# Kernel optimization log

Hardware: AMD Instinct MI355X
Metric: run time of the kernel (lower is better)

## Reference

```python
import jax, jax.numpy as jnp
import numpy as np

Np_, Ny, Nu = 5, 8, 4
NZ = Np_ * (Ny + Nu)  # 60


def setup_inputs() -> dict:
    key = jax.random.key(0)
    ks = jax.random.split(key, 6)
    B, T = 8192, 1024
    u = jax.random.normal(ks[0], (B, T, Nu), dtype=jnp.float32)
    z0 = jax.random.normal(ks[1], (B, NZ), dtype=jnp.float32)
    W1 = jax.random.normal(ks[2], (NZ, 128), dtype=jnp.float32) * (1.0 / np.sqrt(NZ))
    b1 = jnp.zeros((128,), dtype=jnp.float32)
    W2 = jax.random.normal(ks[3], (128, 128), dtype=jnp.float32) * (1.0 / np.sqrt(128))
    b2 = jnp.zeros((128,), dtype=jnp.float32)
    W3 = jax.random.normal(ks[4], (128, Ny), dtype=jnp.float32) * (1.0 / np.sqrt(128))
    b3 = jnp.zeros((Ny,), dtype=jnp.float32)
    return {"u": u, "z0": z0, "W1": W1, "b1": b1, "W2": W2, "b2": b2,
            "W3": W3, "b3": b3}


def reference(u, z0, W1, b1, W2, b2, W3, b3):
    # u: [B, T, Nu], z0: [B, Np*(Ny+Nu)] -> y sequence [B, T, Ny]
    def step(z, u_t):
        h = jnp.tanh(z @ W1 + b1)
        h = jnp.tanh(h @ W2 + b2)
        y = h @ W3 + b3                      # [B, Ny]
        ypseq = z[:, : Np_ * Ny]
        upseq = z[:, Np_ * Ny:]
        z_new = jnp.concatenate(
            (ypseq[:, Ny:], y, upseq[:, Nu:], u_t), axis=-1)
        return z_new, y

    u_tbc = jnp.transpose(u, (1, 0, 2))      # [T, B, Nu]
    _, ys = jax.lax.scan(step, z0, u_tbc)    # ys: [T, B, Ny]
    return jnp.transpose(ys, (1, 0, 2))      # [B, T, Ny]
```

## Files before the change

kernel.cpp:

```cpp
#include <hip/hip_runtime.h>

#define T_STEPS 1024
#define NZV 60
#define H 128
#define NY 8
#define NU 4
#define ZSTR 72
#define HSTR 136

typedef __attribute__((ext_vector_type(8))) short bf16x8;
typedef __attribute__((ext_vector_type(4))) short bf16x4;
typedef __attribute__((ext_vector_type(4))) float f32x4;

__device__ __forceinline__ unsigned short f2bf(float x) {
    unsigned u = __float_as_uint(x);
    u += 0x7FFFu + ((u >> 16) & 1u);
    return (unsigned short)(u >> 16);
}

__device__ __forceinline__ float tanh_fast(float x) {
    float e = __builtin_amdgcn_exp2f(x * 2.8853900817779268f);
    return fmaf(-2.0f, __builtin_amdgcn_rcpf(e + 1.0f), 1.0f);
}

__global__ __launch_bounds__(256, 2)
void cstr_scan_kernel(const float* __restrict__ u_g, const float* __restrict__ z0_g,
                      const float* __restrict__ W1, const float* __restrict__ b1,
                      const float* __restrict__ W2, const float* __restrict__ b2,
                      const float* __restrict__ W3, const float* __restrict__ b3,
                      float* __restrict__ out) {
    __shared__ unsigned short zbuf[2][16][ZSTR];
    __shared__ unsigned short h1s[16][HSTR];
    __shared__ unsigned short h2s[16][HSTR];

    const int tid   = threadIdx.x;
    const int wid   = tid >> 6;
    const int lane  = tid & 63;
    const int b0    = blockIdx.x * 16;
    const int col   = lane & 15;
    const int kg    = lane >> 4;
    const int wrow0 = kg * 4;
    const int urow  = lane >> 2;
    const int uc    = lane & 3;
    const int n0    = wid * 2;

    bf16x8 w1f[2][2], w2f[4][2], w3f[4];
    float b1v[2], b2v[2], b3v;
#pragma unroll
    for (int nl = 0; nl < 2; ++nl) {
        b1v[nl] = b1[(n0 + nl) * 16 + col];
        b2v[nl] = b2[(n0 + nl) * 16 + col];
    }
    b3v = (col < NY) ? b3[col] : 0.f;

#pragma unroll
    for (int kc = 0; kc < 2; ++kc)
#pragma unroll
        for (int nl = 0; nl < 2; ++nl) {
            bf16x8 v;
#pragma unroll
            for (int j = 0; j < 8; ++j) {
                int k = kc * 32 + kg * 8 + j;
                float w = (k < NZV) ? W1[k * H + (n0 + nl) * 16 + col] : 0.f;
                v[j] = (short)f2bf(w);
            }
            w1f[kc][nl] = v;
        }
#pragma unroll
    for (int kc = 0; kc < 4; ++kc)
#pragma unroll
        for (int nl = 0; nl < 2; ++nl) {
            bf16x8 v;
#pragma unroll
            for (int j = 0; j < 8; ++j) {
                int k = kc * 32 + kg * 8 + j;
                v[j] = (short)f2bf(W2[k * H + (n0 + nl) * 16 + col]);
            }
            w2f[kc][nl] = v;
        }
#pragma unroll
    for (int kc = 0; kc < 4; ++kc) {
        bf16x8 v;
#pragma unroll
        for (int j = 0; j < 8; ++j) {
            int k = kc * 32 + kg * 8 + j;
            float w = (col < NY) ? W3[k * NY + col] : 0.f;
            v[j] = (short)f2bf(w);
        }
        w3f[kc] = v;
    }

    {
        unsigned short* zs = &zbuf[0][0][0];
        for (int i = tid; i < 2 * 16 * ZSTR; i += 256) zs[i] = 0;
        __syncthreads();
        for (int i = tid; i < 16 * NZV; i += 256) {
            int r = i / NZV, c = i - r * NZV;
            zbuf[0][r][c] = f2bf(z0_g[(size_t)(b0 + r) * NZV + c]);
        }
        __syncthreads();
    }

    float ureg = 0.f, ureg_n = 0.f;
    if (wid == 3)
        ureg = u_g[(size_t)(b0 + urow) * (T_STEPS * NU) + uc];

    f32x4 yprev = { 0.f, 0.f, 0.f, 0.f };

    int cur = 0;
#pragma unroll 1
    for (int t = 0; t < T_STEPS; ++t) {
        const int nxt = cur ^ 1;

        if (wid == 0 && t > 0 && col < NY) {
#pragma unroll
            for (int r = 0; r < 4; ++r)
                out[(size_t)(b0 + wrow0 + r) * (T_STEPS * NY) + (size_t)(t - 1) * NY + col] = yprev[r];
        }
        if (wid == 3 && t + 1 < T_STEPS)
            ureg_n = u_g[(size_t)(b0 + urow) * (T_STEPS * NU) + (size_t)(t + 1) * NU + uc];

        bf16x8 za[2];
#pragma unroll
        for (int kc = 0; kc < 2; ++kc)
            za[kc] = *(const bf16x8*)&zbuf[cur][col][kc * 32 + kg * 8];
        f32x4 c1[2];
#pragma unroll
        for (int nl = 0; nl < 2; ++nl) {
            f32x4 acc = { b1v[nl], b1v[nl], b1v[nl], b1v[nl] };
            acc = __builtin_amdgcn_mfma_f32_16x16x32_bf16(za[0], w1f[0][nl], acc, 0, 0, 0);
            acc = __builtin_amdgcn_mfma_f32_16x16x32_bf16(za[1], w1f[1][nl], acc, 0, 0, 0);
            c1[nl] = acc;
        }
#pragma unroll
        for (int nl = 0; nl < 2; ++nl)
#pragma unroll
            for (int r = 0; r < 4; ++r)
                h1s[wrow0 + r][(n0 + nl) * 16 + col] = f2bf(tanh_fast(c1[nl][r]));

        if (wid == 3) {
            bf16x4 m0 = *(const bf16x4*)&zbuf[cur][urow][8 + 8 * uc];
            bf16x4 m1 = *(const bf16x4*)&zbuf[cur][urow][12 + 8 * uc];
            bf16x4 m2 = *(const bf16x4*)&zbuf[cur][urow][44 + 4 * uc];
            *(bf16x4*)&zbuf[nxt][urow][8 * uc]      = m0;
            *(bf16x4*)&zbuf[nxt][urow][8 * uc + 4]  = m1;
            *(bf16x4*)&zbuf[nxt][urow][40 + 4 * uc] = m2;
            zbuf[nxt][urow][56 + uc] = f2bf(ureg);
        }
        __syncthreads();

        bf16x8 ha[4];
#pragma unroll
        for (int kc = 0; kc < 4; ++kc)
            ha[kc] = *(const bf16x8*)&h1s[col][kc * 32 + kg * 8];
        f32x4 c2[2];
#pragma unroll
        for (int nl = 0; nl < 2; ++nl) {
            f32x4 a0 = { b2v[nl], b2v[nl], b2v[nl], b2v[nl] };
            f32x4 a1 = { 0.f, 0.f, 0.f, 0.f };
            a0 = __builtin_amdgcn_mfma_f32_16x16x32_bf16(ha[0], w2f[0][nl], a0, 0, 0, 0);
            a1 = __builtin_amdgcn_mfma_f32_16x16x32_bf16(ha[1], w2f[1][nl], a1, 0, 0, 0);
            a0 = __builtin_amdgcn_mfma_f32_16x16x32_bf16(ha[2], w2f[2][nl], a0, 0, 0, 0);
            a1 = __builtin_amdgcn_mfma_f32_16x16x32_bf16(ha[3], w2f[3][nl], a1, 0, 0, 0);
            c2[nl] = a0 + a1;
        }
#pragma unroll
        for (int nl = 0; nl < 2; ++nl)
#pragma unroll
            for (int r = 0; r < 4; ++r)
                h2s[wrow0 + r][(n0 + nl) * 16 + col] = f2bf(tanh_fast(c2[nl][r]));
        __syncthreads();

        if (wid == 0) {
            bf16x8 h2a[4];
#pragma unroll
            for (int kc = 0; kc < 4; ++kc)
                h2a[kc] = *(const bf16x8*)&h2s[col][kc * 32 + kg * 8];
            f32x4 ya = { b3v, b3v, b3v, b3v };
            f32x4 yb = { 0.f, 0.f, 0.f, 0.f };
            ya = __builtin_amdgcn_mfma_f32_16x16x32_bf16(h2a[0], w3f[0], ya, 0, 0, 0);
            yb = __builtin_amdgcn_mfma_f32_16x16x32_bf16(h2a[1], w3f[1], yb, 0, 0, 0);
            ya = __builtin_amdgcn_mfma_f32_16x16x32_bf16(h2a[2], w3f[2], ya, 0, 0, 0);
            yb = __builtin_amdgcn_mfma_f32_16x16x32_bf16(h2a[3], w3f[3], yb, 0, 0, 0);
            f32x4 y = ya + yb;
            if (col < NY) {
#pragma unroll
                for (int r = 0; r < 4; ++r)
                    zbuf[nxt][wrow0 + r][32 + col] = f2bf(y[r]);
            }
            yprev = y;
        }
        __syncthreads();

        cur = nxt;
        ureg = ureg_n;
    }

    if (wid == 0 && (lane & 15) < NY) {
#pragma unroll
        for (int r = 0; r < 4; ++r)
            out[(size_t)(b0 + wrow0 + r) * (T_STEPS * NY) + (size_t)(T_STEPS - 1) * NY + (lane & 15)] = yprev[r];
    }
}

extern "C" void kernel_launch(void* const* d_in, const int* in_sizes, int n_in,
                              void* d_out, int out_size, void* d_ws, size_t ws_size,
                              hipStream_t stream) {
    (void)in_sizes; (void)n_in; (void)d_ws; (void)ws_size; (void)out_size;
    const float* u  = (const float*)d_in[0];
    const float* z0 = (const float*)d_in[1];
    const float* W1 = (const float*)d_in[2];
    const float* b1 = (const float*)d_in[3];
    const float* W2 = (const float*)d_in[4];
    const float* b2 = (const float*)d_in[5];
    const float* W3 = (const float*)d_in[6];
    const float* b3 = (const float*)d_in[7];
    float* out = (float*)d_out;

    dim3 grid(8192 / 16);
    dim3 block(256);
    cstr_scan_kernel<<<grid, block, 0, stream>>>(u, z0, W1, b1, W2, b2, W3, b3, out);
}
```

Baseline: 1.116 ms.

## Split hidden columns across 8 waves and distribute final layer as partial sums

Doubles the block to 512 threads so each of 8 waves owns one 16-column slice of the hidden layers, halving per-wave MFMA work on the serial critical path of each timestep. The output layer is no longer computed by wave 0 alone: every wave multiplies its own h2 slice against its slice of W3 and writes a partial sum to shared memory, which wave 0 then reduces. This shortens the per-step dependency chain at the cost of more waves contending at each barrier, an extra LDS reduction, and some wasted MFMA lanes (half-zero K inputs).

```diff
diff --git a/kernel.cpp b/kernel.cpp
--- a/kernel.cpp
+++ b/kernel.cpp
@@ -23,7 +23,7 @@
     return fmaf(-2.0f, __builtin_amdgcn_rcpf(e + 1.0f), 1.0f);
 }
 
-__global__ __launch_bounds__(256, 2)
+__global__ __launch_bounds__(512, 4)
 void cstr_scan_kernel(const float* __restrict__ u_g, const float* __restrict__ z0_g,
                       const float* __restrict__ W1, const float* __restrict__ b1,
                       const float* __restrict__ W2, const float* __restrict__ b2,
@@ -32,6 +32,7 @@
     __shared__ unsigned short zbuf[2][16][ZSTR];
     __shared__ unsigned short h1s[16][HSTR];
     __shared__ unsigned short h2s[16][HSTR];
+    __shared__ f32x4 ypart[8][64];
 
     const int tid   = threadIdx.x;
     const int wid   = tid >> 6;
@@ -42,59 +43,52 @@
     const int wrow0 = kg * 4;
     const int urow  = lane >> 2;
     const int uc    = lane & 3;
-    const int n0    = wid * 2;
-
-    bf16x8 w1f[2][2], w2f[4][2], w3f[4];
-    float b1v[2], b2v[2], b3v;
-#pragma unroll
-    for (int nl = 0; nl < 2; ++nl) {
-        b1v[nl] = b1[(n0 + nl) * 16 + col];
-        b2v[nl] = b2[(n0 + nl) * 16 + col];
-    }
-    b3v = (col < NY) ? b3[col] : 0.f;
-
-#pragma unroll
-    for (int kc = 0; kc < 2; ++kc)
-#pragma unroll
-        for (int nl = 0; nl < 2; ++nl) {
-            bf16x8 v;
+    const int nbase = wid * 16;
+
+    bf16x8 w1f[2], w2f[4], w3f;
+    const float b1v = b1[nbase + col];
+    const float b2v = b2[nbase + col];
+    const float b3seed = (wid == 0 && col < NY) ? b3[col] : 0.f;
+
+#pragma unroll
+    for (int kc = 0; kc < 2; ++kc) {
+        bf16x8 v;
+#pragma unroll
+        for (int j = 0; j < 8; ++j) {
+            int k = kc * 32 + kg * 8 + j;
+            float w = (k < NZV) ? W1[k * H + nbase + col] : 0.f;
+            v[j] = (short)f2bf(w);
+        }
+        w1f[kc] = v;
+    }
+#pragma unroll
+    for (int kc = 0; kc < 4; ++kc) {
+        bf16x8 v;
+#pragma unroll
+        for (int j = 0; j < 8; ++j) {
+            int k = kc * 32 + kg * 8 + j;
+            v[j] = (short)f2bf(W2[k * H + nbase + col]);
+        }
+        w2f[kc] = v;
+    }
+    {
+        bf16x8 v = { 0, 0, 0, 0, 0, 0, 0, 0 };
+        if (kg < 2) {
 #pragma unroll
             for (int j = 0; j < 8; ++j) {
-                int k = kc * 32 + kg * 8 + j;
-                float w = (k < NZV) ? W1[k * H + (n0 + nl) * 16 + col] : 0.f;
+                int k = nbase + kg * 8 + j;
+                float w = (col < NY) ? W3[k * NY + col] : 0.f;
                 v[j] = (short)f2bf(w);
             }
-            w1f[kc][nl] = v;
-        }
-#pragma unroll
-    for (int kc = 0; kc < 4; ++kc)
-#pragma unroll
-        for (int nl = 0; nl < 2; ++nl) {
-            bf16x8 v;
-#pragma unroll
-            for (int j = 0; j < 8; ++j) {
-                int k = kc * 32 + kg * 8 + j;
-                v[j] = (short)f2bf(W2[k * H + (n0 + nl) * 16 + col]);
-            }
-            w2f[kc][nl] = v;
-        }
-#pragma unroll
-    for (int kc = 0; kc < 4; ++kc) {
-        bf16x8 v;
-#pragma unroll
-        for (int j = 0; j < 8; ++j) {
-            int k = kc * 32 + kg * 8 + j;
-            float w = (col < NY) ? W3[k * NY + col] : 0.f;
-            v[j] = (short)f2bf(w);
-        }
-        w3f[kc] = v;
+        }
+        w3f = v;
     }
 
     {
         unsigned short* zs = &zbuf[0][0][0];
-        for (int i = tid; i < 2 * 16 * ZSTR; i += 256) zs[i] = 0;
-        __syncthreads();
-        for (int i = tid; i < 16 * NZV; i += 256) {
+        for (int i = tid; i < 2 * 16 * ZSTR; i += 512) zs[i] = 0;
+        __syncthreads();
+        for (int i = tid; i < 16 * NZV; i += 512) {
             int r = i / NZV, c = i - r * NZV;
             zbuf[0][r][c] = f2bf(z0_g[(size_t)(b0 + r) * NZV + c]);
         }
@@ -102,7 +96,7 @@
     }
 
     float ureg = 0.f, ureg_n = 0.f;
-    if (wid == 3)
+    if (wid == 7)
         ureg = u_g[(size_t)(b0 + urow) * (T_STEPS * NU) + uc];
 
     f32x4 yprev = { 0.f, 0.f, 0.f, 0.f };
@@ -117,28 +111,19 @@
             for (int r = 0; r < 4; ++r)
                 out[(size_t)(b0 + wrow0 + r) * (T_STEPS * NY) + (size_t)(t - 1) * NY + col] = yprev[r];
         }
-        if (wid == 3 && t + 1 < T_STEPS)
+        if (wid == 7 && t + 1 < T_STEPS)
             ureg_n = u_g[(size_t)(b0 + urow) * (T_STEPS * NU) + (size_t)(t + 1) * NU + uc];
 
-        bf16x8 za[2];
-#pragma unroll
-        for (int kc = 0; kc < 2; ++kc)
-            za[kc] = *(const bf16x8*)&zbuf[cur][col][kc * 32 + kg * 8];
-        f32x4 c1[2];
-#pragma unroll
-        for (int nl = 0; nl < 2; ++nl) {
-            f32x4 acc = { b1v[nl], b1v[nl], b1v[nl], b1v[nl] };
-            acc = __builtin_amdgcn_mfma_f32_16x16x32_bf16(za[0], w1f[0][nl], acc, 0, 0, 0);
-            acc = __builtin_amdgcn_mfma_f32_16x16x32_bf16(za[1], w1f[1][nl], acc, 0, 0, 0);
-            c1[nl] = acc;
-        }
-#pragma unroll
-        for (int nl = 0; nl < 2; ++nl)
-#pragma unroll
-            for (int r = 0; r < 4; ++r)
-                h1s[wrow0 + r][(n0 + nl) * 16 + col] = f2bf(tanh_fast(c1[nl][r]));
-
-        if (wid == 3) {
+        bf16x8 za0 = *(const bf16x8*)&zbuf[cur][col][kg * 8];
+        bf16x8 za1 = *(const bf16x8*)&zbuf[cur][col][32 + kg * 8];
+        f32x4 c1 = { b1v, b1v, b1v, b1v };
+        c1 = __builtin_amdgcn_mfma_f32_16x16x32_bf16(za0, w1f[0], c1, 0, 0, 0);
+        c1 = __builtin_amdgcn_mfma_f32_16x16x32_bf16(za1, w1f[1], c1, 0, 0, 0);
+#pragma unroll
+        for (int r = 0; r < 4; ++r)
+            h1s[wrow0 + r][nbase + col] = f2bf(tanh_fast(c1[r]));
+
+        if (wid == 7) {
             bf16x4 m0 = *(const bf16x4*)&zbuf[cur][urow][8 + 8 * uc];
             bf16x4 m1 = *(const bf16x4*)&zbuf[cur][urow][12 + 8 * uc];
             bf16x4 m2 = *(const bf16x4*)&zbuf[cur][urow][44 + 4 * uc];
@@ -149,46 +134,39 @@
         }
         __syncthreads();
 
-        bf16x8 ha[4];
-#pragma unroll
-        for (int kc = 0; kc < 4; ++kc)
-            ha[kc] = *(const bf16x8*)&h1s[col][kc * 32 + kg * 8];
-        f32x4 c2[2];
-#pragma unroll
-        for (int nl = 0; nl < 2; ++nl) {
-            f32x4 a0 = { b2v[nl], b2v[nl], b2v[nl], b2v[nl] };
-            f32x4 a1 = { 0.f, 0.f, 0.f, 0.f };
-            a0 = __builtin_amdgcn_mfma_f32_16x16x32_bf16(ha[0], w2f[0][nl], a0, 0, 0, 0);
-            a1 = __builtin_amdgcn_mfma_f32_16x16x32_bf16(ha[1], w2f[1][nl], a1, 0, 0, 0);
-            a0 = __builtin_amdgcn_mfma_f32_16x16x32_bf16(ha[2], w2f[2][nl], a0, 0, 0, 0);
-            a1 = __builtin_amdgcn_mfma_f32_16x16x32_bf16(ha[3], w2f[3][nl], a1, 0, 0, 0);
-            c2[nl] = a0 + a1;
-        }
-#pragma unroll
-        for (int nl = 0; nl < 2; ++nl)
-#pragma unroll
-            for (int r = 0; r < 4; ++r)
-                h2s[wrow0 + r][(n0 + nl) * 16 + col] = f2bf(tanh_fast(c2[nl][r]));
+        bf16x8 ha0 = *(const bf16x8*)&h1s[col][0 * 32 + kg * 8];
+        bf16x8 ha1 = *(const bf16x8*)&h1s[col][1 * 32 + kg * 8];
+        bf16x8 ha2 = *(const bf16x8*)&h1s[col][2 * 32 + kg * 8];
+        bf16x8 ha3 = *(const bf16x8*)&h1s[col][3 * 32 + kg * 8];
+        f32x4 a0 = { b2v, b2v, b2v, b2v };
+        f32x4 a1 = { 0.f, 0.f, 0.f, 0.f };
+        a0 = __builtin_amdgcn_mfma_f32_16x16x32_bf16(ha0, w2f[0], a0, 0, 0, 0);
+        a1 = __builtin_amdgcn_mfma_f32_16x16x32_bf16(ha1, w2f[1], a1, 0, 0, 0);
+        a0 = __builtin_amdgcn_mfma_f32_16x16x32_bf16(ha2, w2f[2], a0, 0, 0, 0);
+        a1 = __builtin_amdgcn_mfma_f32_16x16x32_bf16(ha3, w2f[3], a1, 0, 0, 0);
+        f32x4 c2 = a0 + a1;
+#pragma unroll
+        for (int r = 0; r < 4; ++r)
+            h2s[wrow0 + r][nbase + col] = f2bf(tanh_fast(c2[r]));
+
+        bf16x8 af = { 0, 0, 0, 0, 0, 0, 0, 0 };
+        if (kg < 2)
+            af = *(const bf16x8*)&h2s[col][nbase + kg * 8];
+        f32x4 yp = { b3seed, b3seed, b3seed, b3seed };
+        yp = __builtin_amdgcn_mfma_f32_16x16x32_bf16(af, w3f, yp, 0, 0, 0);
+        ypart[wid][lane] = yp;
         __syncthreads();
 
         if (wid == 0) {
-            bf16x8 h2a[4];
-#pragma unroll
-            for (int kc = 0; kc < 4; ++kc)
-                h2a[kc] = *(const bf16x8*)&h2s[col][kc * 32 + kg * 8];
-            f32x4 ya = { b3v, b3v, b3v, b3v };
-            f32x4 yb = { 0.f, 0.f, 0.f, 0.f };
-            ya = __builtin_amdgcn_mfma_f32_16x16x32_bf16(h2a[0], w3f[0], ya, 0, 0, 0);
-            yb = __builtin_amdgcn_mfma_f32_16x16x32_bf16(h2a[1], w3f[1], yb, 0, 0, 0);
-            ya = __builtin_amdgcn_mfma_f32_16x16x32_bf16(h2a[2], w3f[2], ya, 0, 0, 0);
-            yb = __builtin_amdgcn_mfma_f32_16x16x32_bf16(h2a[3], w3f[3], yb, 0, 0, 0);
-            f32x4 y = ya + yb;
+            f32x4 y = ypart[0][lane];
+#pragma unroll
+            for (int w = 1; w < 8; ++w) y = y + ypart[w][lane];
+            yprev = y;
             if (col < NY) {
 #pragma unroll
                 for (int r = 0; r < 4; ++r)
                     zbuf[nxt][wrow0 + r][32 + col] = f2bf(y[r]);
             }
-            yprev = y;
         }
         __syncthreads();
 
@@ -196,10 +174,10 @@
         ureg = ureg_n;
     }
 
-    if (wid == 0 && (lane & 15) < NY) {
+    if (wid == 0 && col < NY) {
 #pragma unroll
         for (int r = 0; r < 4; ++r)
-            out[(size_t)(b0 + wrow0 + r) * (T_STEPS * NY) + (size_t)(T_STEPS - 1) * NY + (lane & 15)] = yprev[r];
+            out[(size_t)(b0 + wrow0 + r) * (T_STEPS * NY) + (size_t)(T_STEPS - 1) * NY + col] = yprev[r];
     }
 }
 
@@ -218,6 +196,6 @@
     float* out = (float*)d_out;
 
     dim3 grid(8192 / 16);
-    dim3 block(256);
+    dim3 block(512);
     cstr_scan_kernel<<<grid, block, 0, stream>>>(u, z0, W1, b1, W2, b2, W3, b3, out);
 }
```

After: 1.288 ms. 15.4% more time.

## Fold output layer into next step's first layer to drop a barrier

Applied to the files above, without the earlier changes.

Precomputes W3·W1[y rows] as a fused weight so the first-layer pre-activation of step t reads the previous step's h2 directly, instead of waiting for y to be computed and written back into z. y is now computed off the critical path by wave 0, in parallel with the first-layer MFMAs. This cuts one __syncthreads per timestep (three to two). In exchange it adds MFMAs per step (K=128 instead of 8 for the y contribution) and a double-buffered h2 array, and the product W3·W1 rounded to bf16 changes numerics slightly.

```diff
diff --git a/kernel.cpp b/kernel.cpp
--- a/kernel.cpp
+++ b/kernel.cpp
@@ -31,7 +31,7 @@
                       float* __restrict__ out) {
     __shared__ unsigned short zbuf[2][16][ZSTR];
     __shared__ unsigned short h1s[16][HSTR];
-    __shared__ unsigned short h2s[16][HSTR];
+    __shared__ unsigned short h2s[2][16][HSTR];
 
     const int tid   = threadIdx.x;
     const int wid   = tid >> 6;
@@ -42,14 +42,19 @@
     const int wrow0 = kg * 4;
     const int urow  = lane >> 2;
     const int uc    = lane & 3;
-    const int n0    = wid * 2;
-
-    bf16x8 w1f[2][2], w2f[4][2], w3f[4];
-    float b1v[2], b2v[2], b3v;
+    const int nbase = wid * 32;
+
+    bf16x8 w1f[2][2], w1yx[2], w4f[4][2], w2f[4][2], w3f[4];
+    float b1v[2], b1e[2], b2v[2], b3v;
 #pragma unroll
     for (int nl = 0; nl < 2; ++nl) {
-        b1v[nl] = b1[(n0 + nl) * 16 + col];
-        b2v[nl] = b2[(n0 + nl) * 16 + col];
+        const int n = nbase + nl * 16 + col;
+        b1v[nl] = b1[n];
+        float corr = 0.f;
+#pragma unroll
+        for (int m = 0; m < NY; ++m) corr += b3[m] * W1[(32 + m) * H + n];
+        b1e[nl] = b1v[nl] + corr;
+        b2v[nl] = b2[n];
     }
     b3v = (col < NY) ? b3[col] : 0.f;
 
@@ -57,25 +62,54 @@
     for (int kc = 0; kc < 2; ++kc)
 #pragma unroll
         for (int nl = 0; nl < 2; ++nl) {
+            const int n = nbase + nl * 16 + col;
             bf16x8 v;
 #pragma unroll
             for (int j = 0; j < 8; ++j) {
                 int k = kc * 32 + kg * 8 + j;
-                float w = (k < NZV) ? W1[k * H + (n0 + nl) * 16 + col] : 0.f;
+                float w = (k < NZV && !(k >= 32 && k < 40)) ? W1[k * H + n] : 0.f;
                 v[j] = (short)f2bf(w);
             }
             w1f[kc][nl] = v;
         }
 #pragma unroll
+    for (int nl = 0; nl < 2; ++nl) {
+        const int n = nbase + nl * 16 + col;
+        bf16x8 v;
+#pragma unroll
+        for (int j = 0; j < 8; ++j) {
+            int k = 32 + kg * 8 + j;
+            float w = (k < 40) ? W1[k * H + n] : 0.f;
+            v[j] = (short)f2bf(w);
+        }
+        w1yx[nl] = v;
+    }
+#pragma unroll
     for (int kc = 0; kc < 4; ++kc)
 #pragma unroll
         for (int nl = 0; nl < 2; ++nl) {
+            const int n = nbase + nl * 16 + col;
             bf16x8 v;
 #pragma unroll
             for (int j = 0; j < 8; ++j) {
                 int k = kc * 32 + kg * 8 + j;
-                v[j] = (short)f2bf(W2[k * H + (n0 + nl) * 16 + col]);
+                float acc = 0.f;
+#pragma unroll
+                for (int m = 0; m < NY; ++m)
+                    acc += W3[k * NY + m] * W1[(32 + m) * H + n];
+                v[j] = (short)f2bf(acc);
             }
+            w4f[kc][nl] = v;
+        }
+#pragma unroll
+    for (int kc = 0; kc < 4; ++kc)
+#pragma unroll
+        for (int nl = 0; nl < 2; ++nl) {
+            const int n = nbase + nl * 16 + col;
+            bf16x8 v;
+#pragma unroll
+            for (int j = 0; j < 8; ++j)
+                v[j] = (short)f2bf(W2[(kc * 32 + kg * 8 + j) * H + n]);
             w2f[kc][nl] = v;
         }
 #pragma unroll
@@ -93,6 +127,8 @@
     {
         unsigned short* zs = &zbuf[0][0][0];
         for (int i = tid; i < 2 * 16 * ZSTR; i += 256) zs[i] = 0;
+        unsigned short* hs = &h2s[0][0][0];
+        for (int i = tid; i < 2 * 16 * HSTR; i += 256) hs[i] = 0;
         __syncthreads();
         for (int i = tid; i < 16 * NZV; i += 256) {
             int r = i / NZV, c = i - r * NZV;
@@ -105,39 +141,74 @@
     if (wid == 3)
         ureg = u_g[(size_t)(b0 + urow) * (T_STEPS * NU) + uc];
 
-    f32x4 yprev = { 0.f, 0.f, 0.f, 0.f };
-
-    int cur = 0;
+    int cur = 0, ph = 0;
 #pragma unroll 1
     for (int t = 0; t < T_STEPS; ++t) {
         const int nxt = cur ^ 1;
 
-        if (wid == 0 && t > 0 && col < NY) {
-#pragma unroll
-            for (int r = 0; r < 4; ++r)
-                out[(size_t)(b0 + wrow0 + r) * (T_STEPS * NY) + (size_t)(t - 1) * NY + col] = yprev[r];
-        }
         if (wid == 3 && t + 1 < T_STEPS)
             ureg_n = u_g[(size_t)(b0 + urow) * (T_STEPS * NU) + (size_t)(t + 1) * NU + uc];
 
-        bf16x8 za[2];
-#pragma unroll
-        for (int kc = 0; kc < 2; ++kc)
-            za[kc] = *(const bf16x8*)&zbuf[cur][col][kc * 32 + kg * 8];
-        f32x4 c1[2];
-#pragma unroll
-        for (int nl = 0; nl < 2; ++nl) {
-            f32x4 acc = { b1v[nl], b1v[nl], b1v[nl], b1v[nl] };
-            acc = __builtin_amdgcn_mfma_f32_16x16x32_bf16(za[0], w1f[0][nl], acc, 0, 0, 0);
-            acc = __builtin_amdgcn_mfma_f32_16x16x32_bf16(za[1], w1f[1][nl], acc, 0, 0, 0);
-            c1[nl] = acc;
-        }
-#pragma unroll
-        for (int nl = 0; nl < 2; ++nl)
+        bf16x8 za0 = *(const bf16x8*)&zbuf[cur][col][kg * 8];
+        bf16x8 za1 = *(const bf16x8*)&zbuf[cur][col][32 + kg * 8];
+        bf16x8 hp0 = *(const bf16x8*)&h2s[ph][col][0 * 32 + kg * 8];
+        bf16x8 hp1 = *(const bf16x8*)&h2s[ph][col][1 * 32 + kg * 8];
+        bf16x8 hp2 = *(const bf16x8*)&h2s[ph][col][2 * 32 + kg * 8];
+        bf16x8 hp3 = *(const bf16x8*)&h2s[ph][col][3 * 32 + kg * 8];
+#pragma unroll
+        for (int nl = 0; nl < 2; ++nl) {
+            float seed = t ? b1e[nl] : b1v[nl];
+            f32x4 s0 = { seed, seed, seed, seed };
+            f32x4 s1 = { 0.f, 0.f, 0.f, 0.f };
+            s0 = __builtin_amdgcn_mfma_f32_16x16x32_bf16(za0, w1f[0][nl], s0, 0, 0, 0);
+            s1 = __builtin_amdgcn_mfma_f32_16x16x32_bf16(hp0, w4f[0][nl], s1, 0, 0, 0);
+            s0 = __builtin_amdgcn_mfma_f32_16x16x32_bf16(za1, w1f[1][nl], s0, 0, 0, 0);
+            s1 = __builtin_amdgcn_mfma_f32_16x16x32_bf16(hp1, w4f[1][nl], s1, 0, 0, 0);
+            s0 = __builtin_amdgcn_mfma_f32_16x16x32_bf16(hp2, w4f[2][nl], s0, 0, 0, 0);
+            s1 = __builtin_amdgcn_mfma_f32_16x16x32_bf16(hp3, w4f[3][nl], s1, 0, 0, 0);
+            if (t == 0)
+                s0 = __builtin_amdgcn_mfma_f32_16x16x32_bf16(za1, w1yx[nl], s0, 0, 0, 0);
+            f32x4 c1 = s0 + s1;
 #pragma unroll
             for (int r = 0; r < 4; ++r)
-                h1s[wrow0 + r][(n0 + nl) * 16 + col] = f2bf(tanh_fast(c1[nl][r]));
-
+                h1s[wrow0 + r][nbase + nl * 16 + col] = f2bf(tanh_fast(c1[r]));
+        }
+        if (wid == 0 && t > 0) {
+            f32x4 ya = { b3v, b3v, b3v, b3v };
+            f32x4 yb = { 0.f, 0.f, 0.f, 0.f };
+            ya = __builtin_amdgcn_mfma_f32_16x16x32_bf16(hp0, w3f[0], ya, 0, 0, 0);
+            yb = __builtin_amdgcn_mfma_f32_16x16x32_bf16(hp1, w3f[1], yb, 0, 0, 0);
+            ya = __builtin_amdgcn_mfma_f32_16x16x32_bf16(hp2, w3f[2], ya, 0, 0, 0);
+            yb = __builtin_amdgcn_mfma_f32_16x16x32_bf16(hp3, w3f[3], yb, 0, 0, 0);
+            f32x4 y = ya + yb;
+            if (col < NY) {
+#pragma unroll
+                for (int r = 0; r < 4; ++r)
+                    zbuf[cur][wrow0 + r][32 + col] = f2bf(y[r]);
+#pragma unroll
+                for (int r = 0; r < 4; ++r)
+                    out[(size_t)(b0 + wrow0 + r) * (T_STEPS * NY) + (size_t)(t - 1) * NY + col] = y[r];
+            }
+        }
+        __syncthreads();
+
+        bf16x8 ha0 = *(const bf16x8*)&h1s[col][0 * 32 + kg * 8];
+        bf16x8 ha1 = *(const bf16x8*)&h1s[col][1 * 32 + kg * 8];
+        bf16x8 ha2 = *(const bf16x8*)&h1s[col][2 * 32 + kg * 8];
+        bf16x8 ha3 = *(const bf16x8*)&h1s[col][3 * 32 + kg * 8];
+#pragma unroll
+        for (int nl = 0; nl < 2; ++nl) {
+            f32x4 a0 = { b2v[nl], b2v[nl], b2v[nl], b2v[nl] };
+            f32x4 a1 = { 0.f, 0.f, 0.f, 0.f };
+            a0 = __builtin_amdgcn_mfma_f32_16x16x32_bf16(ha0, w2f[0][nl], a0, 0, 0, 0);
+            a1 = __builtin_amdgcn_mfma_f32_16x16x32_bf16(ha1, w2f[1][nl], a1, 0, 0, 0);
+            a0 = __builtin_amdgcn_mfma_f32_16x16x32_bf16(ha2, w2f[2][nl], a0, 0, 0, 0);
+            a1 = __builtin_amdgcn_mfma_f32_16x16x32_bf16(ha3, w2f[3][nl], a1, 0, 0, 0);
+            f32x4 c2 = a0 + a1;
+#pragma unroll
+            for (int r = 0; r < 4; ++r)
+                h2s[ph ^ 1][wrow0 + r][nbase + nl * 16 + col] = f2bf(tanh_fast(c2[r]));
+        }
         if (wid == 3) {
             bf16x4 m0 = *(const bf16x4*)&zbuf[cur][urow][8 + 8 * uc];
             bf16x4 m1 = *(const bf16x4*)&zbuf[cur][urow][12 + 8 * uc];
@@ -149,57 +220,28 @@
         }
         __syncthreads();
 
-        bf16x8 ha[4];
-#pragma unroll
-        for (int kc = 0; kc < 4; ++kc)
-            ha[kc] = *(const bf16x8*)&h1s[col][kc * 32 + kg * 8];
-        f32x4 c2[2];
-#pragma unroll
-        for (int nl = 0; nl < 2; ++nl) {
-            f32x4 a0 = { b2v[nl], b2v[nl], b2v[nl], b2v[nl] };
-            f32x4 a1 = { 0.f, 0.f, 0.f, 0.f };
-            a0 = __builtin_amdgcn_mfma_f32_16x16x32_bf16(ha[0], w2f[0][nl], a0, 0, 0, 0);
-            a1 = __builtin_amdgcn_mfma_f32_16x16x32_bf16(ha[1], w2f[1][nl], a1, 0, 0, 0);
-            a0 = __builtin_amdgcn_mfma_f32_16x16x32_bf16(ha[2], w2f[2][nl], a0, 0, 0, 0);
-            a1 = __builtin_amdgcn_mfma_f32_16x16x32_bf16(ha[3], w2f[3][nl], a1, 0, 0, 0);
-            c2[nl] = a0 + a1;
-        }
-#pragma unroll
-        for (int nl = 0; nl < 2; ++nl)
+        cur = nxt;
+        ph ^= 1;
+        ureg = ureg_n;
+    }
+
+    if (wid == 0) {
+        bf16x8 hp0 = *(const bf16x8*)&h2s[ph][col][0 * 32 + kg * 8];
+        bf16x8 hp1 = *(const bf16x8*)&h2s[ph][col][1 * 32 + kg * 8];
+        bf16x8 hp2 = *(const bf16x8*)&h2s[ph][col][2 * 32 + kg * 8];
+        bf16x8 hp3 = *(const bf16x8*)&h2s[ph][col][3 * 32 + kg * 8];
+        f32x4 ya = { b3v, b3v, b3v, b3v };
+        f32x4 yb = { 0.f, 0.f, 0.f, 0.f };
+        ya = __builtin_amdgcn_mfma_f32_16x16x32_bf16(hp0, w3f[0], ya, 0, 0, 0);
+        yb = __builtin_amdgcn_mfma_f32_16x16x32_bf16(hp1, w3f[1], yb, 0, 0, 0);
+        ya = __builtin_amdgcn_mfma_f32_16x16x32_bf16(hp2, w3f[2], ya, 0, 0, 0);
+        yb = __builtin_amdgcn_mfma_f32_16x16x32_bf16(hp3, w3f[3], yb, 0, 0, 0);
+        f32x4 y = ya + yb;
+        if (col < NY) {
 #pragma unroll
             for (int r = 0; r < 4; ++r)
-                h2s[wrow0 + r][(n0 + nl) * 16 + col] = f2bf(tanh_fast(c2[nl][r]));
-        __syncthreads();
-
-        if (wid == 0) {
-            bf16x8 h2a[4];
-#pragma unroll
-            for (int kc = 0; kc < 4; ++kc)
-                h2a[kc] = *(const bf16x8*)&h2s[col][kc * 32 + kg * 8];
-            f32x4 ya = { b3v, b3v, b3v, b3v };
-            f32x4 yb = { 0.f, 0.f, 0.f, 0.f };
-            ya = __builtin_amdgcn_mfma_f32_16x16x32_bf16(h2a[0], w3f[0], ya, 0, 0, 0);
-            yb = __builtin_amdgcn_mfma_f32_16x16x32_bf16(h2a[1], w3f[1], yb, 0, 0, 0);
-            ya = __builtin_amdgcn_mfma_f32_16x16x32_bf16(h2a[2], w3f[2], ya, 0, 0, 0);
-            yb = __builtin_amdgcn_mfma_f32_16x16x32_bf16(h2a[3], w3f[3], yb, 0, 0, 0);
-            f32x4 y = ya + yb;
-            if (col < NY) {
-#pragma unroll
-                for (int r = 0; r < 4; ++r)
-                    zbuf[nxt][wrow0 + r][32 + col] = f2bf(y[r]);
-            }
-            yprev = y;
-        }
-        __syncthreads();
-
-        cur = nxt;
-        ureg = ureg_n;
-    }
-
-    if (wid == 0 && (lane & 15) < NY) {
-#pragma unroll
-        for (int r = 0; r < 4; ++r)
-            out[(size_t)(b0 + wrow0 + r) * (T_STEPS * NY) + (size_t)(T_STEPS - 1) * NY + (lane & 15)] = yprev[r];
+                out[(size_t)(b0 + wrow0 + r) * (T_STEPS * NY) + (size_t)(T_STEPS - 1) * NY + col] = y[r];
+        }
     }
 }
 
```

Result: slower. 1.332 ms (+19.4%).

## Batch y outputs in LDS and flush coalesced every 16 steps, unroll by two

Applied to the files above, without the earlier changes.

Instead of wave 0 writing scattered 4-byte y stores to global memory every step, y values are staged in a shared ybuf for 16 timesteps and then all 256 threads write them out as contiguous 16-byte vectors per batch row. The step loop is unrolled by two so the double-buffer index becomes a compile-time constant. f32-to-bf16 conversion now uses the packed v_cvt_pk_bf16_f32 instruction in place of the manual rounding. The trade is extra LDS and a flush phase every 16 steps, which relies on the barrier at the end of each step to make ybuf visible to all threads.

```diff
diff --git a/kernel.cpp b/kernel.cpp
--- a/kernel.cpp
+++ b/kernel.cpp
@@ -16,6 +16,12 @@
     unsigned u = __float_as_uint(x);
     u += 0x7FFFu + ((u >> 16) & 1u);
     return (unsigned short)(u >> 16);
+}
+
+__device__ __forceinline__ unsigned cvt_pk_bf16(float lo, float hi) {
+    unsigned r;
+    asm("v_cvt_pk_bf16_f32 %0, %1, %2" : "=v"(r) : "v"(lo), "v"(hi));
+    return r;
 }
 
 __device__ __forceinline__ float tanh_fast(float x) {
@@ -32,6 +38,7 @@
     __shared__ unsigned short zbuf[2][16][ZSTR];
     __shared__ unsigned short h1s[16][HSTR];
     __shared__ unsigned short h2s[16][HSTR];
+    __shared__ float ybuf[16][16][NY];
 
     const int tid   = threadIdx.x;
     const int wid   = tid >> 6;
@@ -42,14 +49,14 @@
     const int wrow0 = kg * 4;
     const int urow  = lane >> 2;
     const int uc    = lane & 3;
-    const int n0    = wid * 2;
+    const int nbase = wid * 32;
 
     bf16x8 w1f[2][2], w2f[4][2], w3f[4];
     float b1v[2], b2v[2], b3v;
 #pragma unroll
     for (int nl = 0; nl < 2; ++nl) {
-        b1v[nl] = b1[(n0 + nl) * 16 + col];
-        b2v[nl] = b2[(n0 + nl) * 16 + col];
+        b1v[nl] = b1[nbase + nl * 16 + col];
+        b2v[nl] = b2[nbase + nl * 16 + col];
     }
     b3v = (col < NY) ? b3[col] : 0.f;
 
@@ -61,7 +68,7 @@
 #pragma unroll
             for (int j = 0; j < 8; ++j) {
                 int k = kc * 32 + kg * 8 + j;
-                float w = (k < NZV) ? W1[k * H + (n0 + nl) * 16 + col] : 0.f;
+                float w = (k < NZV) ? W1[k * H + nbase + nl * 16 + col] : 0.f;
                 v[j] = (short)f2bf(w);
             }
             w1f[kc][nl] = v;
@@ -74,7 +81,7 @@
 #pragma unroll
             for (int j = 0; j < 8; ++j) {
                 int k = kc * 32 + kg * 8 + j;
-                v[j] = (short)f2bf(W2[k * H + (n0 + nl) * 16 + col]);
+                v[j] = (short)f2bf(W2[k * H + nbase + nl * 16 + col]);
             }
             w2f[kc][nl] = v;
         }
@@ -101,106 +108,121 @@
         __syncthreads();
     }
 
+    const float* uptr = u_g + (size_t)(b0 + urow) * (T_STEPS * NU) + uc;
     float ureg = 0.f, ureg_n = 0.f;
-    if (wid == 3)
-        ureg = u_g[(size_t)(b0 + urow) * (T_STEPS * NU) + uc];
-
-    f32x4 yprev = { 0.f, 0.f, 0.f, 0.f };
-
-    int cur = 0;
+    if (wid == 3) ureg = *uptr;
+
+    int t = 0;
+
+#define STEP_BODY(CUR)                                                                  \
+    {                                                                                   \
+        const int nxt = (CUR) ^ 1;                                                      \
+                                    \
+        bf16x8 za0 = *(const bf16x8*)&zbuf[CUR][col][kg * 8];                           \
+        bf16x8 za1 = *(const bf16x8*)&zbuf[CUR][col][32 + kg * 8];                      \
+        _Pragma("unroll")                                                               \
+        for (int nl = 0; nl < 2; ++nl) {                                                \
+            f32x4 c1 = { b1v[nl], b1v[nl], b1v[nl], b1v[nl] };                          \
+            c1 = __builtin_amdgcn_mfma_f32_16x16x32_bf16(za0, w1f[0][nl], c1, 0, 0, 0); \
+            c1 = __builtin_amdgcn_mfma_f32_16x16x32_bf16(za1, w1f[1][nl], c1, 0, 0, 0); \
+            unsigned p01 = cvt_pk_bf16(tanh_fast(c1[0]), tanh_fast(c1[1]));             \
+            unsigned p23 = cvt_pk_bf16(tanh_fast(c1[2]), tanh_fast(c1[3]));             \
+            const int n = nbase + nl * 16 + col;                                        \
+            h1s[wrow0 + 0][n] = (unsigned short)p01;                                    \
+            h1s[wrow0 + 1][n] = (unsigned short)(p01 >> 16);                            \
+            h1s[wrow0 + 2][n] = (unsigned short)p23;                                    \
+            h1s[wrow0 + 3][n] = (unsigned short)(p23 >> 16);                            \
+        }                                                                               \
+                \
+        if (wid == 3) {                                                                 \
+            bf16x4 m0 = *(const bf16x4*)&zbuf[CUR][urow][8 + 8 * uc];                   \
+            bf16x4 m1 = *(const bf16x4*)&zbuf[CUR][urow][12 + 8 * uc];                  \
+            bf16x4 m2 = *(const bf16x4*)&zbuf[CUR][urow][44 + 4 * uc];                  \
+            *(bf16x4*)&zbuf[nxt][urow][8 * uc]      = m0;                               \
+            *(bf16x4*)&zbuf[nxt][urow][8 * uc + 4]  = m1;                               \
+            *(bf16x4*)&zbuf[nxt][urow][40 + 4 * uc] = m2;                               \
+            zbuf[nxt][urow][56 + uc] = f2bf(ureg);                                      \
+            uptr += NU;                                                                 \
+            if (t + 1 < T_STEPS) ureg_n = *uptr;                                        \
+        }                                                                               \
+        __syncthreads();                      \
+                                              \
+        bf16x8 ha0 = *(const bf16x8*)&h1s[col][0 * 32 + kg * 8];                        \
+        bf16x8 ha1 = *(const bf16x8*)&h1s[col][1 * 32 + kg * 8];                        \
+        bf16x8 ha2 = *(const bf16x8*)&h1s[col][2 * 32 + kg * 8];                        \
+        bf16x8 ha3 = *(const bf16x8*)&h1s[col][3 * 32 + kg * 8];                        \
+        _Pragma("unroll")                                                               \
+        for (int nl = 0; nl < 2; ++nl) {                                                \
+            f32x4 a0 = { b2v[nl], b2v[nl], b2v[nl], b2v[nl] };                          \
+            f32x4 a1 = { 0.f, 0.f, 0.f, 0.f };                                          \
+            a0 = __builtin_amdgcn_mfma_f32_16x16x32_bf16(ha0, w2f[0][nl], a0, 0, 0, 0); \
+            a1 = __builtin_amdgcn_mfma_f32_16x16x32_bf16(ha1, w2f[1][nl], a1, 0, 0, 0); \
+            a0 = __builtin_amdgcn_mfma_f32_16x16x32_bf16(ha2, w2f[2][nl], a0, 0, 0, 0); \
+            a1 = __builtin_amdgcn_mfma_f32_16x16x32_bf16(ha3, w2f[3][nl], a1, 0, 0, 0); \
+            f32x4 c2 = a0 + a1;                                                         \
+            unsigned p01 = cvt_pk_bf16(tanh_fast(c2[0]), tanh_fast(c2[1]));             \
+            unsigned p23 = cvt_pk_bf16(tanh_fast(c2[2]), tanh_fast(c2[3]));             \
+            const int n = nbase + nl * 16 + col;                                        \
+            h2s[wrow0 + 0][n] = (unsigned short)p01;                                    \
+            h2s[wrow0 + 1][n] = (unsigned short)(p01 >> 16);                            \
+            h2s[wrow0 + 2][n] = (unsigned short)p23;                                    \
+            h2s[wrow0 + 3][n] = (unsigned short)(p23 >> 16);                            \
+        }                                                                               \
+        __syncthreads();                                              \
+                              \
+        if (wid == 0) {                                                                 \
+            bf16x8 hp0 = *(const bf16x8*)&h2s[col][0 * 32 + kg * 8];                    \
+            bf16x8 hp1 = *(const bf16x8*)&h2s[col][1 * 32 + kg * 8];                    \
+            bf16x8 hp2 = *(const bf16x8*)&h2s[col][2 * 32 + kg * 8];                    \
+            bf16x8 hp3 = *(const bf16x8*)&h2s[col][3 * 32 + kg * 8];                    \
+            f32x4 ya = { b3v, b3v, b3v, b3v };                                          \
+            f32x4 yb = { 0.f, 0.f, 0.f, 0.f };                                          \
+            ya = __builtin_amdgcn_mfma_f32_16x16x32_bf16(hp0, w3f[0], ya, 0, 0, 0);     \
+            yb = __builtin_amdgcn_mfma_f32_16x16x32_bf16(hp1, w3f[1], yb, 0, 0, 0);     \
+            ya = __builtin_amdgcn_mfma_f32_16x16x32_bf16(hp2, w3f[2], ya, 0, 0, 0);     \
+            yb = __builtin_amdgcn_mfma_f32_16x16x32_bf16(hp3, w3f[3], yb, 0, 0, 0);     \
+            f32x4 y = ya + yb;                                                          \
+            if (col < NY) {                                                             \
+                unsigned q01 = cvt_pk_bf16(y[0], y[1]);                                 \
+                unsigned q23 = cvt_pk_bf16(y[2], y[3]);                                 \
+                zbuf[nxt][wrow0 + 0][32 + col] = (unsigned short)q01;                   \
+                zbuf[nxt][wrow0 + 1][32 + col] = (unsigned short)(q01 >> 16);           \
+                zbuf[nxt][wrow0 + 2][32 + col] = (unsigned short)q23;                   \
+                zbuf[nxt][wrow0 + 3][32 + col] = (unsigned short)(q23 >> 16);           \
+                const int ts = t & 15;                                                  \
+                ybuf[ts][wrow0 + 0][col] = y[0];                                        \
+                ybuf[ts][wrow0 + 1][col] = y[1];                                        \
+                ybuf[ts][wrow0 + 2][col] = y[2];                                        \
+                ybuf[ts][wrow0 + 3][col] = y[3];                                        \
+            }                                                                           \
+        }                                                                               \
+        __syncthreads();               \
+        ureg = ureg_n;                                                                  \
+        ++t;                                                                            \
+    }
+
+    const int frow  = tid >> 4;
+    const int ftoff = tid & 15;
+
+#define FLUSH(BASE_T)                                                                   \
+    {                                                                                   \
+        const f32x4* yp = (const f32x4*)&ybuf[ftoff][frow][0];                          \
+        f32x4 v0 = yp[0], v1 = yp[1];                                                   \
+        float* op = out + ((size_t)(b0 + frow) * T_STEPS + (BASE_T) + ftoff) * NY;      \
+        *(f32x4*)op = v0;                                                               \
+        *(f32x4*)(op + 4) = v1;                                                         \
+    }
+
 #pragma unroll 1
-    for (int t = 0; t < T_STEPS; ++t) {
-        const int nxt = cur ^ 1;
-
-        if (wid == 0 && t > 0 && col < NY) {
-#pragma unroll
-            for (int r = 0; r < 4; ++r)
-                out[(size_t)(b0 + wrow0 + r) * (T_STEPS * NY) + (size_t)(t - 1) * NY + col] = yprev[r];
-        }
-        if (wid == 3 && t + 1 < T_STEPS)
-            ureg_n = u_g[(size_t)(b0 + urow) * (T_STEPS * NU) + (size_t)(t + 1) * NU + uc];
-
-        bf16x8 za[2];
-#pragma unroll
-        for (int kc = 0; kc < 2; ++kc)
-            za[kc] = *(const bf16x8*)&zbuf[cur][col][kc * 32 + kg * 8];
-        f32x4 c1[2];
-#pragma unroll
-        for (int nl = 0; nl < 2; ++nl) {
-            f32x4 acc = { b1v[nl], b1v[nl], b1v[nl], b1v[nl] };
-            acc = __builtin_amdgcn_mfma_f32_16x16x32_bf16(za[0], w1f[0][nl], acc, 0, 0, 0);
-            acc = __builtin_amdgcn_mfma_f32_16x16x32_bf16(za[1], w1f[1][nl], acc, 0, 0, 0);
-            c1[nl] = acc;
-        }
-#pragma unroll
-        for (int nl = 0; nl < 2; ++nl)
-#pragma unroll
-            for (int r = 0; r < 4; ++r)
-                h1s[wrow0 + r][(n0 + nl) * 16 + col] = f2bf(tanh_fast(c1[nl][r]));
-
-        if (wid == 3) {
-            bf16x4 m0 = *(const bf16x4*)&zbuf[cur][urow][8 + 8 * uc];
-            bf16x4 m1 = *(const bf16x4*)&zbuf[cur][urow][12 + 8 * uc];
-            bf16x4 m2 = *(const bf16x4*)&zbuf[cur][urow][44 + 4 * uc];
-            *(bf16x4*)&zbuf[nxt][urow][8 * uc]      = m0;
-            *(bf16x4*)&zbuf[nxt][urow][8 * uc + 4]  = m1;
-            *(bf16x4*)&zbuf[nxt][urow][40 + 4 * uc] = m2;
-            zbuf[nxt][urow][56 + uc] = f2bf(ureg);
-        }
-        __syncthreads();
-
-        bf16x8 ha[4];
-#pragma unroll
-        for (int kc = 0; kc < 4; ++kc)
-            ha[kc] = *(const bf16x8*)&h1s[col][kc * 32 + kg * 8];
-        f32x4 c2[2];
-#pragma unroll
-        for (int nl = 0; nl < 2; ++nl) {
-            f32x4 a0 = { b2v[nl], b2v[nl], b2v[nl], b2v[nl] };
-            f32x4 a1 = { 0.f, 0.f, 0.f, 0.f };
-            a0 = __builtin_amdgcn_mfma_f32_16x16x32_bf16(ha[0], w2f[0][nl], a0, 0, 0, 0);
-            a1 = __builtin_amdgcn_mfma_f32_16x16x32_bf16(ha[1], w2f[1][nl], a1, 0, 0, 0);
-            a0 = __builtin_amdgcn_mfma_f32_16x16x32_bf16(ha[2], w2f[2][nl], a0, 0, 0, 0);
-            a1 = __builtin_amdgcn_mfma_f32_16x16x32_bf16(ha[3], w2f[3][nl], a1, 0, 0, 0);
-            c2[nl] = a0 + a1;
-        }
-#pragma unroll
-        for (int nl = 0; nl < 2; ++nl)
-#pragma unroll
-            for (int r = 0; r < 4; ++r)
-                h2s[wrow0 + r][(n0 + nl) * 16 + col] = f2bf(tanh_fast(c2[nl][r]));
-        __syncthreads();
-
-        if (wid == 0) {
-            bf16x8 h2a[4];
-#pragma unroll
-            for (int kc = 0; kc < 4; ++kc)
-                h2a[kc] = *(const bf16x8*)&h2s[col][kc * 32 + kg * 8];
-            f32x4 ya = { b3v, b3v, b3v, b3v };
-            f32x4 yb = { 0.f, 0.f, 0.f, 0.f };
-            ya = __builtin_amdgcn_mfma_f32_16x16x32_bf16(h2a[0], w3f[0], ya, 0, 0, 0);
-            yb = __builtin_amdgcn_mfma_f32_16x16x32_bf16(h2a[1], w3f[1], yb, 0, 0, 0);
-            ya = __builtin_amdgcn_mfma_f32_16x16x32_bf16(h2a[2], w3f[2], ya, 0, 0, 0);
-            yb = __builtin_amdgcn_mfma_f32_16x16x32_bf16(h2a[3], w3f[3], yb, 0, 0, 0);
-            f32x4 y = ya + yb;
-            if (col < NY) {
-#pragma unroll
-                for (int r = 0; r < 4; ++r)
-                    zbuf[nxt][wrow0 + r][32 + col] = f2bf(y[r]);
-            }
-            yprev = y;
-        }
-        __syncthreads();
-
-        cur = nxt;
-        ureg = ureg_n;
-    }
-
-    if (wid == 0 && (lane & 15) < NY) {
-#pragma unroll
-        for (int r = 0; r < 4; ++r)
-            out[(size_t)(b0 + wrow0 + r) * (T_STEPS * NY) + (size_t)(T_STEPS - 1) * NY + (lane & 15)] = yprev[r];
-    }
+    for (int it = 0; it < T_STEPS / 2; ++it) {
+        if ((t & 15) == 0 && t > 0)
+            FLUSH(t - 16);
+        STEP_BODY(0)
+        STEP_BODY(1)
+    }
+    FLUSH(T_STEPS - 16);
+#undef STEP_BODY
+#undef FLUSH
 }
 
 extern "C" void kernel_launch(void* const* d_in, const int* in_sizes, int n_in,
```

Result: faster. 1.083 ms (-3.0%).
